# Performance work log

Hardware: AMD Instinct MI355X
Metric: run time of the kernel (lower is better)

## Reference

```python
import jax, jax.numpy as jnp
import numpy as np

B, S, D = 2, 2048, 2048
H = 16
Q_LORA, KV_LORA = 1536, 512
D_NOPE, D_ROPE, D_V = 128, 64, 128
QK_D = D_NOPE + D_ROPE  # 192
EPS = 1e-6
ROPE_THETA = 10000.0


def rms_norm(x, w, eps=EPS):
    return x * jax.lax.rsqrt(jnp.mean(x * x, axis=-1, keepdims=True) + eps) * w


def apply_rope(x, cos, sin):
    # x: [b, s, h, d]; cos/sin: [s, d//2]; pairs are interleaved (x0,x1),(x2,x3),...
    xr, xi = x[..., 0::2], x[..., 1::2]
    c = cos[None, :, None, :]
    s = sin[None, :, None, :]
    yr = xr * c - xi * s
    yi = xr * s + xi * c
    return jnp.stack([yr, yi], axis=-1).reshape(x.shape)


def setup_inputs() -> dict:
    key = jax.random.key(0)
    ks = jax.random.split(key, 8)
    sd = 0.02
    pos = jnp.arange(S, dtype=jnp.float32)
    inv_freq = 1.0 / (ROPE_THETA ** (jnp.arange(0, D_ROPE, 2, dtype=jnp.float32) / D_ROPE))
    ang = pos[:, None] * inv_freq[None, :]  # [S, D_ROPE//2]
    mask = jnp.triu(jnp.full((S, S), float('-inf'), dtype=jnp.float32), k=1)
    return {
        'x': jax.random.normal(ks[0], (B, S, D), dtype=jnp.float32),
        'freqs_cos': jnp.cos(ang),
        'freqs_sin': jnp.sin(ang),
        'mask': mask,
        'wq_a': jax.random.normal(ks[1], (Q_LORA, D), dtype=jnp.float32) * sd,
        'q_norm_w': jnp.ones((Q_LORA,), dtype=jnp.float32),
        'wq_b': jax.random.normal(ks[2], (H * QK_D, Q_LORA), dtype=jnp.float32) * sd,
        'wkv_a': jax.random.normal(ks[3], (KV_LORA + D_ROPE, D), dtype=jnp.float32) * sd,
        'kv_norm_w': jnp.ones((KV_LORA,), dtype=jnp.float32),
        'wkv_b': jax.random.normal(ks[4], (H * (D_NOPE + D_V), KV_LORA), dtype=jnp.float32) * sd,
        'wo': jax.random.normal(ks[5], (D, H * D_V), dtype=jnp.float32) * sd,
    }


def reference(x, freqs_cos, freqs_sin, mask, wq_a, q_norm_w, wq_b, wkv_a, kv_norm_w, wkv_b, wo):
    b, s, _ = x.shape
    # query path: down-proj -> RMSNorm -> up-proj
    q = rms_norm(x @ wq_a.T, q_norm_w) @ wq_b.T          # [b, s, H*QK_D]
    q = q.reshape(b, s, H, QK_D)
    q_nope, q_pe = q[..., :D_NOPE], q[..., D_NOPE:]
    q_pe = apply_rope(q_pe, freqs_cos, freqs_sin)
    # kv path: joint down-proj, split latent / rope key
    kv_full = x @ wkv_a.T                                 # [b, s, KV_LORA + D_ROPE]
    kv, k_pe = kv_full[..., :KV_LORA], kv_full[..., KV_LORA:]
    k_pe = apply_rope(k_pe[:, :, None, :], freqs_cos, freqs_sin)  # [b, s, 1, D_ROPE]
    q = jnp.concatenate([q_nope, q_pe], axis=-1)          # [b, s, H, QK_D]
    kv = rms_norm(kv, kv_norm_w) @ wkv_b.T                # [b, s, H*(D_NOPE+D_V)]
    kv = kv.reshape(b, s, H, D_NOPE + D_V)
    k_nope, v = kv[..., :D_NOPE], kv[..., D_NOPE:]
    k = jnp.concatenate([k_nope, jnp.broadcast_to(k_pe, (b, s, H, D_ROPE))], axis=-1)
    scale = QK_D ** -0.5
    scores = jnp.einsum('bshd,bthd->bsht', q, k) * scale + mask[None, :, None, :]
    probs = jax.nn.softmax(scores.astype(jnp.float32), axis=-1).astype(x.dtype)
    out = jnp.einsum('bsht,bthd->bshd', probs, v).reshape(b, s, H * D_V)
    return out @ wo.T
```

## Files before the change

### kernel.cpp

```cpp
#include <hip/hip_runtime.h>
#include <hip/hip_bf16.h>

typedef __bf16 bf16_t;
typedef __bf16 bf16x8 __attribute__((ext_vector_type(8)));
typedef __bf16 bf16x4 __attribute__((ext_vector_type(4)));
typedef __bf16 bf16x2 __attribute__((ext_vector_type(2)));
typedef float  f32x4  __attribute__((ext_vector_type(4)));
typedef float  f32x16 __attribute__((ext_vector_type(16)));

#define NB 2
#define NS 2048
#define ND 2048
#define NH 16
#define QLORA 1536
#define KVLORA 512
#define DNOPE 128
#define DROPE 64
#define DVDIM 128
#define QKD 192

#define QSCALE 0.10411754f

#if __has_builtin(__builtin_amdgcn_exp2f)
#define EXP2F(x) __builtin_amdgcn_exp2f(x)
#else
#define EXP2F(x) __expf((x) * 0.69314718056f)
#endif
#if __has_builtin(__builtin_amdgcn_rcpf)
#define RCPF(x) __builtin_amdgcn_rcpf(x)
#else
#define RCPF(x) (1.0f / (x))
#endif

typedef __attribute__((address_space(3))) void as3_void;
typedef __attribute__((address_space(1))) const void as1_void;
__device__ __forceinline__ void gload16(const void* g, void* l) {
  __builtin_amdgcn_global_load_lds((as1_void*)g, (as3_void*)l, 16, 0, 0);
}

__device__ __forceinline__ int pack2(float a, float b) {
  bf16x2 t = {(bf16_t)a, (bf16_t)b};
  return __builtin_bit_cast(int, t);
}

__global__ __launch_bounds__(256) void k_cvt_all(
    const float* __restrict__ x, const float* __restrict__ wqa,
    const float* __restrict__ wqb, const float* __restrict__ wkva,
    const float* __restrict__ wkvb, const float* __restrict__ wo,
    bf16_t* __restrict__ xb, bf16_t* __restrict__ wqab, bf16_t* __restrict__ wqbb,
    bf16_t* __restrict__ wkvab, bf16_t* __restrict__ wkvbb, bf16_t* __restrict__ wob) {
  const int c0 = 2097152, c1 = 2883584, c2 = 4063232, c3 = 4358144, c4 = 4882432,
            c5 = 5931008;
  int i = blockIdx.x * 256 + threadIdx.x;
  for (; i < c5; i += gridDim.x * 256) {
    const float* src;
    bf16_t* dst;
    int off;
    if (i < c0) { src = x; dst = xb; off = i; }
    else if (i < c1) { src = wqa; dst = wqab; off = i - c0; }
    else if (i < c2) { src = wqb; dst = wqbb; off = i - c1; }
    else if (i < c3) { src = wkva; dst = wkvab; off = i - c2; }
    else if (i < c4) { src = wkvb; dst = wkvbb; off = i - c3; }
    else { src = wo; dst = wob; off = i - c4; }
    float4 v = reinterpret_cast<const float4*>(src)[off];
    bf16x4 o = {(bf16_t)v.x, (bf16_t)v.y, (bf16_t)v.z, (bf16_t)v.w};
    reinterpret_cast<bf16x4*>(dst)[off] = o;
  }
}

template <int EPI>
__device__ __forceinline__ void gemm_core(
    int rank, bf16_t* As, bf16_t* Bs,
    const bf16_t* __restrict__ A, const bf16_t* __restrict__ Bw,
    float* __restrict__ Cf, float* __restrict__ Cf2,
    bf16_t* __restrict__ Kout, bf16_t* __restrict__ Vtout,
    const float* __restrict__ fc, const float* __restrict__ fs,
    int M, int N, int K) {
  const int tid = threadIdx.x;
  const int lane = tid & 63;
  const int wave = tid >> 6;
  const int wm = (wave >> 1) * 64, wn = (wave & 1) * 64;
  const int nxt = (N + 127) >> 7;
  const int by = rank / nxt, bx = rank - by * nxt;
  const int m0 = by * 128, n0 = bx * 128;
  const int l15 = lane & 15, l4 = lane >> 4;
  const int srow = lane >> 3;
  const int scol = ((lane & 7) ^ srow) * 8;

  const f32x4 Z4 = {0.f, 0.f, 0.f, 0.f};
  f32x4 acc[4][4];
#pragma unroll
  for (int i = 0; i < 4; ++i)
#pragma unroll
    for (int j = 0; j < 4; ++j) acc[i][j] = Z4;

  auto stage = [&](int buf, int k0) {
#pragma unroll
    for (int c = 0; c < 4; ++c) {
      int chunk = c * 4 + wave;
      int row = chunk * 8 + srow;
      gload16(A + (size_t)(m0 + row) * K + k0 + scol, &As[buf * 8192 + chunk * 512]);
      gload16(Bw + (size_t)(n0 + row) * K + k0 + scol, &Bs[buf * 8192 + chunk * 512]);
    }
  };

  const int nk = K >> 6;
  stage(0, 0);
  int cur = 0;
#pragma unroll 1
  for (int t = 0; t < nk; ++t) {
    if (t + 1 < nk) {
      stage(cur ^ 1, (t + 1) * 64);
      asm volatile("s_waitcnt vmcnt(8)" ::: "memory");
    } else {
      asm volatile("s_waitcnt vmcnt(0)" ::: "memory");
    }
    __builtin_amdgcn_sched_barrier(0);
    __builtin_amdgcn_s_barrier();
    __builtin_amdgcn_sched_barrier(0);
#pragma unroll
    for (int ks = 0; ks < 2; ++ks) {
      int kc = ks * 4 + l4;
      int pc = (kc ^ (l15 & 7)) * 8;
      bf16x8 af[4], bfr[4];
#pragma unroll
      for (int f = 0; f < 4; ++f) {
        af[f] = *reinterpret_cast<const bf16x8*>(
            &As[cur * 8192 + (wm + f * 16 + l15) * 64 + pc]);
        bfr[f] = *reinterpret_cast<const bf16x8*>(
            &Bs[cur * 8192 + (wn + f * 16 + l15) * 64 + pc]);
      }
#pragma unroll
      for (int fi = 0; fi < 4; ++fi)
#pragma unroll
        for (int fj = 0; fj < 4; ++fj)
          acc[fi][fj] = __builtin_amdgcn_mfma_f32_16x16x32_bf16(af[fi], bfr[fj], acc[fi][fj], 0, 0, 0);
    }
    __builtin_amdgcn_sched_barrier(0);
    __builtin_amdgcn_s_barrier();
    cur ^= 1;
  }

#pragma unroll
  for (int fi = 0; fi < 4; ++fi) {
#pragma unroll
    for (int fj = 0; fj < 4; ++fj) {
      int col = n0 + wn + fj * 16 + l15;
      int row0 = m0 + wm + fi * 16 + l4 * 4;
      if (EPI == 1) {
        int h = col >> 8, rr = col & 255;
        int b = row0 >> 11, s0 = row0 & 2047;
        if (rr < DNOPE) {
#pragma unroll
          for (int r = 0; r < 4; ++r)
            Kout[(((size_t)(b * NH + h)) * NS + s0 + r) * QKD + rr] =
                (bf16_t)acc[fi][fj][r];
        } else {
          bf16x4 pv4 = {(bf16_t)acc[fi][fj][0], (bf16_t)acc[fi][fj][1],
                        (bf16_t)acc[fi][fj][2], (bf16_t)acc[fi][fj][3]};
          *reinterpret_cast<bf16x4*>(
              &Vtout[(((size_t)(b * NH + h)) * DVDIM + (rr - DNOPE)) * NS + s0]) = pv4;
        }
      } else {
#pragma unroll
        for (int r = 0; r < 4; ++r) {
          int row = row0 + r;
          float v = acc[fi][fj][r];
          if (EPI == 0) {
            Cf[(size_t)row * N + col] = v;
          } else if (EPI == 2) {
            int h = col / 192;
            int d = col - h * 192;
            int b = row >> 11, s = row & 2047;
            float y = v;
            if (d >= DNOPE) {
              float pv = __shfl_xor(v, 1);
              int pp = ((d & ~1) - DNOPE) >> 1;
              float c = fc[s * 32 + pp], si = fs[s * 32 + pp];
              y = (col & 1) ? (pv * si + v * c) : (v * c - pv * si);
            }
            Kout[((size_t)(b * NH + h) * NS + s) * QKD + d] = (bf16_t)(y * QSCALE);
          } else {
            if (col < QLORA) Cf[(size_t)row * QLORA + col] = v;
            else if (col < QLORA + KVLORA + DROPE)
              Cf2[(size_t)row * (KVLORA + DROPE) + (col - QLORA)] = v;
          }
        }
      }
    }
  }
}

template <int EPI>
__global__ __launch_bounds__(256) void k_gemm_bt(
    const bf16_t* __restrict__ A, const bf16_t* __restrict__ Bw,
    float* __restrict__ Cf, float* __restrict__ Cf2,
    bf16_t* __restrict__ Kout, bf16_t* __restrict__ Vtout,
    const float* __restrict__ fc, const float* __restrict__ fs,
    int M, int N, int K) {
  __shared__ bf16_t As[2 * 128 * 64];
  __shared__ bf16_t Bs[2 * 128 * 64];
  const int per = gridDim.x >> 3;
  const int rank = (blockIdx.x & 7) * per + (blockIdx.x >> 3);
  gemm_core<EPI>(rank, As, Bs, A, Bw, Cf, Cf2, Kout, Vtout, fc, fs, M, N, K);
}

__global__ __launch_bounds__(256) void k_gemm_dual(
    const bf16_t* __restrict__ A2, const bf16_t* __restrict__ B2,
    bf16_t* __restrict__ Qb, const float* __restrict__ fc,
    const float* __restrict__ fs, const bf16_t* __restrict__ A1,
    const bf16_t* __restrict__ B1, bf16_t* __restrict__ Kout,
    bf16_t* __restrict__ Vtout) {
  __shared__ bf16_t As[2 * 128 * 64];
  __shared__ bf16_t Bs[2 * 128 * 64];
  const int G2 = 768;
  if ((int)blockIdx.x < G2) {
    int id = blockIdx.x;
    int rank = (id & 7) * (G2 >> 3) + (id >> 3);
    gemm_core<2>(rank, As, Bs, A2, B2, nullptr, nullptr, Qb, nullptr, fc, fs,
                 NB * NS, NH * QKD, QLORA);
  } else {
    int id = blockIdx.x - G2;
    int rank = (id & 7) * (1024 >> 3) + (id >> 3);
    gemm_core<1>(rank, As, Bs, A1, B1, nullptr, nullptr, Kout, Vtout, nullptr,
                 nullptr, NB * NS, NH * (DNOPE + DVDIM), KVLORA);
  }
}

__global__ __launch_bounds__(256) void k_norm_post(
    const float* __restrict__ qa, const float* __restrict__ qw,
    bf16_t* __restrict__ qan, const float* __restrict__ kvf,
    const float* __restrict__ kw, const float* __restrict__ fc,
    const float* __restrict__ fs, bf16_t* __restrict__ kvn,
    bf16_t* __restrict__ Kb) {
  int row = blockIdx.x;
  __shared__ float red[4];
  {
    const float* rp = qa + (size_t)row * QLORA;
    float ss = 0.f;
    for (int c = threadIdx.x * 4; c < QLORA; c += 1024) {
      float4 v = *reinterpret_cast<const float4*>(rp + c);
      ss += v.x * v.x + v.y * v.y + v.z * v.z + v.w * v.w;
    }
#pragma unroll
    for (int m = 32; m; m >>= 1) ss += __shfl_xor(ss, m);
    if ((threadIdx.x & 63) == 0) red[threadIdx.x >> 6] = ss;
    __syncthreads();
    float tot = red[0] + red[1] + red[2] + red[3];
    float rs = rsqrtf(tot / (float)QLORA + 1e-6f);
    for (int c = threadIdx.x * 4; c < QLORA; c += 1024) {
      float4 v = *reinterpret_cast<const float4*>(rp + c);
      bf16x4 o = {(bf16_t)(v.x * rs * qw[c]), (bf16_t)(v.y * rs * qw[c + 1]),
                  (bf16_t)(v.z * rs * qw[c + 2]), (bf16_t)(v.w * rs * qw[c + 3])};
      *reinterpret_cast<bf16x4*>(qan + (size_t)row * QLORA + c) = o;
    }
  }
  __syncthreads();
  const float* rp = kvf + (size_t)row * (KVLORA + DROPE);
  float ss = 0.f;
  float4 v = {0.f, 0.f, 0.f, 0.f};
  if (threadIdx.x < 128) {
    v = reinterpret_cast<const float4*>(rp)[threadIdx.x];
    ss = v.x * v.x + v.y * v.y + v.z * v.z + v.w * v.w;
  }
#pragma unroll
  for (int m = 32; m; m >>= 1) ss += __shfl_xor(ss, m);
  if ((threadIdx.x & 63) == 0) red[threadIdx.x >> 6] = ss;
  __syncthreads();
  float tot = red[0] + red[1] + red[2] + red[3];
  float rs = rsqrtf(tot / (float)KVLORA + 1e-6f);
  if (threadIdx.x < 128) {
    int c = threadIdx.x * 4;
    bf16x4 o = {(bf16_t)(v.x * rs * kw[c]), (bf16_t)(v.y * rs * kw[c + 1]),
                (bf16_t)(v.z * rs * kw[c + 2]), (bf16_t)(v.w * rs * kw[c + 3])};
    *reinterpret_cast<bf16x4*>(kvn + (size_t)row * KVLORA + c) = o;
  }
  int b = row >> 11, s = row & 2047;
  if (threadIdx.x < 32) {
    int p = threadIdx.x;
    float x0 = rp[KVLORA + 2 * p], x1 = rp[KVLORA + 2 * p + 1];
    float c = fc[s * 32 + p], si = fs[s * 32 + p];
    float yr = x0 * c - x1 * si, yi = x0 * si + x1 * c;
    bf16_t br = (bf16_t)yr, bi = (bf16_t)yi;
    for (int h = 0; h < NH; ++h) {
      size_t ob = ((size_t)(b * NH + h) * NS + s) * QKD + DNOPE;
      Kb[ob + 2 * p] = br;
      Kb[ob + 2 * p + 1] = bi;
    }
  }
}

__global__ __launch_bounds__(256, 2) void k_attn(const bf16_t* __restrict__ Qb,
                                                 const bf16_t* __restrict__ Kb,
                                                 const bf16_t* __restrict__ Vtb,
                                                 bf16_t* __restrict__ Ao) {
  __shared__ bf16x8 Ks8[2][64 * 24];
  __shared__ bf16x8 Vs8[2][128 * 8];
  const int id = blockIdx.x;
  const int bh = id & 31;
  const int aa = (id >> 5) & 7;
  const int qt = (id >> 8) ? aa : (15 - aa);
  const int b = bh >> 4, h = bh & 15;
  const int tid = threadIdx.x;
  const int lane = tid & 63, wave = tid >> 6;
  const int l31 = lane & 31, hi = lane >> 5;
  const int q0w = qt * 128 + wave * 32;
  const int qg = q0w + l31;
  const int c4 = hi * 4;
  const int ntiles = 2 * qt + 2;
  const size_t bhNS = (size_t)bh * NS;

  const bf16_t* KbB = Kb + bhNS * QKD;
  const bf16_t* VtB = Vtb + (size_t)bh * DVDIM * NS;
  int koff[6], voff[4];
#pragma unroll
  for (int i = 0; i < 6; ++i) {
    int p = tid + i * 256;
    int row = p / 24, pc = p % 24;
    int lc = (pc & ~7) | ((pc ^ row) & 7);
    koff[i] = row * QKD + lc * 8;
  }
#pragma unroll
  for (int i = 0; i < 4; ++i) {
    int p = tid + i * 256;
    int row = p >> 3, pc = p & 7;
    int lc = pc ^ (row & 7);
    voff[i] = row * NS + lc * 8;
  }

  auto stageKV = [&](int buf, int kv0) {
    const bf16_t* ksrc = KbB + kv0 * QKD;
    const bf16_t* vsrc = VtB + kv0;
    bf16x8* kdst = &Ks8[buf][wave * 64];
    bf16x8* vdst = &Vs8[buf][wave * 64];
#pragma unroll
    for (int i = 0; i < 6; ++i) gload16(ksrc + koff[i], kdst + i * 256);
#pragma unroll
    for (int i = 0; i < 4; ++i) gload16(vsrc + voff[i], vdst + i * 256);
  };

  bf16x8 qf[12];
  {
    const bf16_t* qp = Qb + (bhNS + qg) * QKD + hi * 8;
#pragma unroll
    for (int ks = 0; ks < 12; ++ks)
      qf[ks] = *reinterpret_cast<const bf16x8*>(qp + ks * 16);
  }

  f32x16 oacc[4];
#pragma unroll
  for (int d = 0; d < 4; ++d) oacc[d] = {};
  float mrun = -3e38f, lrun = 0.f;

  stageKV(0, 0);
  int cur = 0;

#pragma unroll 1
  for (int kt = 0; kt < ntiles; ++kt) {
    const int kv0 = kt * 64;
    if (kt + 1 < ntiles) {
      stageKV(cur ^ 1, kv0 + 64);
      asm volatile("s_waitcnt vmcnt(10)" ::: "memory");
    } else {
      asm volatile("s_waitcnt vmcnt(0)" ::: "memory");
    }
    __builtin_amdgcn_sched_barrier(0);
    __builtin_amdgcn_s_barrier();
    __builtin_amdgcn_sched_barrier(0);

    if (kv0 <= q0w + 31) {
      f32x16 sacc[2];
      sacc[0] = {};
      sacc[1] = {};
#pragma unroll
      for (int ks = 0; ks < 12; ++ks) {
#pragma unroll
        for (int kh = 0; kh < 2; ++kh) {
          int row = kh * 32 + l31;
          int c = ks * 2 + hi;
          int pc = (c & ~7) | ((c ^ row) & 7);
          sacc[kh] = __builtin_amdgcn_mfma_f32_32x32x16_bf16(Ks8[cur][row * 24 + pc],
                                                             qf[ks], sacc[kh], 0, 0, 0);
        }
      }

      const bool diag = (kv0 + 63 > q0w);
      float mloc = -3e38f;
#pragma unroll
      for (int kh = 0; kh < 2; ++kh)
#pragma unroll
        for (int rg = 0; rg < 16; ++rg) {
          float s = sacc[kh][rg];
          if (diag) {
            int kg = kv0 + kh * 32 + (rg & 3) + 8 * (rg >> 2) + c4;
            if (kg > qg) s = -3e38f;
            sacc[kh][rg] = s;
          }
          mloc = fmaxf(mloc, s);
        }
      mloc = fmaxf(mloc, __shfl_xor(mloc, 32));

      if (!__all(mloc <= mrun)) {
        float mn = fmaxf(mrun, mloc);
        float fac = EXP2F(mrun - mn);
        mrun = mn;
        lrun *= fac;
#pragma unroll
        for (int d = 0; d < 4; ++d)
#pragma unroll
          for (int rg = 0; rg < 16; ++rg) oacc[d][rg] *= fac;
      }

      float rsum = 0.f;
      int W[8][2];
#pragma unroll
      for (int kh = 0; kh < 2; ++kh)
#pragma unroll
        for (int g = 0; g < 4; ++g) {
          float p0 = EXP2F(sacc[kh][4 * g + 0] - mrun);
          float p1 = EXP2F(sacc[kh][4 * g + 1] - mrun);
          float p2 = EXP2F(sacc[kh][4 * g + 2] - mrun);
          float p3 = EXP2F(sacc[kh][4 * g + 3] - mrun);
          rsum += (p0 + p1) + (p2 + p3);
          W[kh * 4 + g][0] = pack2(p0, p1);
          W[kh * 4 + g][1] = pack2(p2, p3);
        }
      rsum += __shfl_xor(rsum, 32);
      lrun += rsum;

      bf16x8 pa[4];
#pragma unroll
      for (int pks = 0; pks < 4; ++pks) {
        int kh = pks >> 1, G0 = (pks & 1) * 2;
        int a0 = W[kh * 4 + G0][0], a1 = W[kh * 4 + G0][1];
        int b0 = W[kh * 4 + G0 + 1][0], b1 = W[kh * 4 + G0 + 1][1];
        int own0 = hi ? b0 : a0, own1 = hi ? b1 : a1;
        int oth0 = hi ? a0 : b0, oth1 = hi ? a1 : b1;
        int rc0 = __shfl_xor(oth0, 32), rc1 = __shfl_xor(oth1, 32);
        int4 wv;
        wv.x = hi ? rc0 : own0;
        wv.y = hi ? rc1 : own1;
        wv.z = hi ? own0 : rc0;
        wv.w = hi ? own1 : rc1;
        pa[pks] = __builtin_bit_cast(bf16x8, wv);
      }

#pragma unroll
      for (int pks = 0; pks < 4; ++pks)
#pragma unroll
        for (int dvt = 0; dvt < 4; ++dvt) {
          int row = dvt * 32 + l31;
          int pc = (pks * 2 + hi) ^ (row & 7);
          oacc[dvt] = __builtin_amdgcn_mfma_f32_32x32x16_bf16(Vs8[cur][row * 8 + pc],
                                                              pa[pks], oacc[dvt], 0, 0, 0);
        }
    }

    __builtin_amdgcn_sched_barrier(0);
    __builtin_amdgcn_s_barrier();
    cur ^= 1;
  }

  float lr = RCPF(lrun);
  bf16_t* base = Ao + ((size_t)(b * NS) + qg) * (NH * DVDIM) + h * DVDIM;
#pragma unroll
  for (int dvt = 0; dvt < 4; ++dvt)
#pragma unroll
    for (int rg4 = 0; rg4 < 4; ++rg4) {
      int dv0 = dvt * 32 + 8 * rg4 + c4;
      bf16x4 o = {(bf16_t)(oacc[dvt][rg4 * 4 + 0] * lr),
                  (bf16_t)(oacc[dvt][rg4 * 4 + 1] * lr),
                  (bf16_t)(oacc[dvt][rg4 * 4 + 2] * lr),
                  (bf16_t)(oacc[dvt][rg4 * 4 + 3] * lr)};
      *reinterpret_cast<bf16x4*>(base + dv0) = o;
    }
}

extern "C" void kernel_launch(void* const* d_in, const int* in_sizes, int n_in,
                              void* d_out, int out_size, void* d_ws, size_t ws_size,
                              hipStream_t stream) {
  (void)in_sizes; (void)n_in; (void)out_size; (void)ws_size;
  const float* x = (const float*)d_in[0];
  const float* fcos = (const float*)d_in[1];
  const float* fsin = (const float*)d_in[2];
  const float* wq_a = (const float*)d_in[4];
  const float* q_norm_w = (const float*)d_in[5];
  const float* wq_b = (const float*)d_in[6];
  const float* wkv_a = (const float*)d_in[7];
  const float* kv_norm_w = (const float*)d_in[8];
  const float* wkv_b = (const float*)d_in[9];
  const float* wo = (const float*)d_in[10];
  float* out = (float*)d_out;

  char* p = (char*)d_ws;
  bf16_t* x_bf = (bf16_t*)(p);
  bf16_t* wqa_bf = (bf16_t*)(p + 16777216);
  bf16_t* wkva_bf = (bf16_t*)(p + 23068672);
  bf16_t* wqb_bf = (bf16_t*)(p + 25427968);
  bf16_t* wkvb_bf = (bf16_t*)(p + 34865152);
  bf16_t* wo_bf = (bf16_t*)(p + 39059456);
  float* qa_f32 = (float*)(p + 47448064);
  bf16_t* Kb = (bf16_t*)(p + 47448064);
  bf16_t* qan_bf = (bf16_t*)(p + 72613888);
  bf16_t* Qb = (bf16_t*)(p + 85196800);
  char* r2 = p + 110362624;
  float* kvf_f32 = (float*)(r2);
  bf16_t* kvn_bf = (bf16_t*)(r2 + 9437184);
  bf16_t* Vtb = (bf16_t*)(r2 + 13631488);
  bf16_t* attn_bf = (bf16_t*)(r2 + 30408704);

  k_cvt_all<<<2048, 256, 0, stream>>>(x, wq_a, wq_b, wkv_a, wkv_b, wo, x_bf, wqa_bf,
                                      wqb_bf, wkva_bf, wkvb_bf, wo_bf);

  k_gemm_bt<3><<<dim3(544), 256, 0, stream>>>(x_bf, wqa_bf, qa_f32, kvf_f32,
                                              nullptr, nullptr, nullptr, nullptr,
                                              NB * NS, QLORA + KVLORA + DROPE, ND);
  k_norm_post<<<NB * NS, 256, 0, stream>>>(qa_f32, q_norm_w, qan_bf, kvf_f32,
                                           kv_norm_w, fcos, fsin, kvn_bf, Kb);
  k_gemm_dual<<<dim3(1792), 256, 0, stream>>>(qan_bf, wqb_bf, Qb, fcos, fsin,
                                              kvn_bf, wkvb_bf, Kb, Vtb);
  k_attn<<<dim3(512), 256, 0, stream>>>(Qb, Kb, Vtb, attn_bf);
  k_gemm_bt<0><<<dim3(512), 256, 0, stream>>>(attn_bf, wo_bf, out, nullptr, nullptr,
                                              nullptr, nullptr, nullptr, NB * NS, ND,
                                              NH * DVDIM);
}
```

Baseline: 321.2 us.

## Use 256x128 tiles with 512-thread blocks for the dual up-projection GEMM

Adds a gemm_core256 variant that computes 256x128 output tiles with 8 waves, each keeping a 64x64 accumulator, and moves the existing epilogue into a shared gemm_epi helper. k_gemm_dual now launches 896 blocks of 512 threads instead of 1792 blocks of 256. Each B tile loaded into shared memory is reused across twice as many rows, which halves the B-operand global and LDS traffic per output. In exchange the block uses 48KB of LDS and needs more threads per block, which may lower occupancy and leaves fewer blocks to balance across the CUs.

```diff
diff --git a/kernel.cpp b/kernel.cpp
--- a/kernel.cpp
+++ b/kernel.cpp
@@ -69,6 +69,52 @@
 }
 
 template <int EPI>
+__device__ __forceinline__ void gemm_epi(
+    int col, int row0, const f32x4& a4,
+    float* __restrict__ Cf, float* __restrict__ Cf2,
+    bf16_t* __restrict__ Kout, bf16_t* __restrict__ Vtout,
+    const float* __restrict__ fc, const float* __restrict__ fs, int N) {
+  if (EPI == 1) {
+    int h = col >> 8, rr = col & 255;
+    int b = row0 >> 11, s0 = row0 & 2047;
+    if (rr < DNOPE) {
+#pragma unroll
+      for (int r = 0; r < 4; ++r)
+        Kout[(((size_t)(b * NH + h)) * NS + s0 + r) * QKD + rr] = (bf16_t)a4[r];
+    } else {
+      bf16x4 pv4 = {(bf16_t)a4[0], (bf16_t)a4[1], (bf16_t)a4[2], (bf16_t)a4[3]};
+      *reinterpret_cast<bf16x4*>(
+          &Vtout[(((size_t)(b * NH + h)) * DVDIM + (rr - DNOPE)) * NS + s0]) = pv4;
+    }
+  } else {
+#pragma unroll
+    for (int r = 0; r < 4; ++r) {
+      int row = row0 + r;
+      float v = a4[r];
+      if (EPI == 0) {
+        Cf[(size_t)row * N + col] = v;
+      } else if (EPI == 2) {
+        int h = col / 192;
+        int d = col - h * 192;
+        int b = row >> 11, s = row & 2047;
+        float y = v;
+        if (d >= DNOPE) {
+          float pv = __shfl_xor(v, 1);
+          int pp = ((d & ~1) - DNOPE) >> 1;
+          float c = fc[s * 32 + pp], si = fs[s * 32 + pp];
+          y = (col & 1) ? (pv * si + v * c) : (v * c - pv * si);
+        }
+        Kout[((size_t)(b * NH + h) * NS + s) * QKD + d] = (bf16_t)(y * QSCALE);
+      } else {
+        if (col < QLORA) Cf[(size_t)row * QLORA + col] = v;
+        else if (col < QLORA + KVLORA + DROPE)
+          Cf2[(size_t)row * (KVLORA + DROPE) + (col - QLORA)] = v;
+      }
+    }
+  }
+}
+
+template <int EPI>
 __device__ __forceinline__ void gemm_core(
     int rank, bf16_t* As, bf16_t* Bs,
     const bf16_t* __restrict__ A, const bf16_t* __restrict__ Bw,
@@ -142,53 +188,97 @@
   }
 
 #pragma unroll
-  for (int fi = 0; fi < 4; ++fi) {
-#pragma unroll
-    for (int fj = 0; fj < 4; ++fj) {
-      int col = n0 + wn + fj * 16 + l15;
-      int row0 = m0 + wm + fi * 16 + l4 * 4;
-      if (EPI == 1) {
-        int h = col >> 8, rr = col & 255;
-        int b = row0 >> 11, s0 = row0 & 2047;
-        if (rr < DNOPE) {
-#pragma unroll
-          for (int r = 0; r < 4; ++r)
-            Kout[(((size_t)(b * NH + h)) * NS + s0 + r) * QKD + rr] =
-                (bf16_t)acc[fi][fj][r];
-        } else {
-          bf16x4 pv4 = {(bf16_t)acc[fi][fj][0], (bf16_t)acc[fi][fj][1],
-                        (bf16_t)acc[fi][fj][2], (bf16_t)acc[fi][fj][3]};
-          *reinterpret_cast<bf16x4*>(
-              &Vtout[(((size_t)(b * NH + h)) * DVDIM + (rr - DNOPE)) * NS + s0]) = pv4;
-        }
-      } else {
-#pragma unroll
-        for (int r = 0; r < 4; ++r) {
-          int row = row0 + r;
-          float v = acc[fi][fj][r];
-          if (EPI == 0) {
-            Cf[(size_t)row * N + col] = v;
-          } else if (EPI == 2) {
-            int h = col / 192;
-            int d = col - h * 192;
-            int b = row >> 11, s = row & 2047;
-            float y = v;
-            if (d >= DNOPE) {
-              float pv = __shfl_xor(v, 1);
-              int pp = ((d & ~1) - DNOPE) >> 1;
-              float c = fc[s * 32 + pp], si = fs[s * 32 + pp];
-              y = (col & 1) ? (pv * si + v * c) : (v * c - pv * si);
-            }
-            Kout[((size_t)(b * NH + h) * NS + s) * QKD + d] = (bf16_t)(y * QSCALE);
-          } else {
-            if (col < QLORA) Cf[(size_t)row * QLORA + col] = v;
-            else if (col < QLORA + KVLORA + DROPE)
-              Cf2[(size_t)row * (KVLORA + DROPE) + (col - QLORA)] = v;
-          }
-        }
+  for (int fi = 0; fi < 4; ++fi)
+#pragma unroll
+    for (int fj = 0; fj < 4; ++fj)
+      gemm_epi<EPI>(n0 + wn + fj * 16 + l15, m0 + wm + fi * 16 + l4 * 4, acc[fi][fj],
+                    Cf, Cf2, Kout, Vtout, fc, fs, N);
+}
+
+template <int EPI>
+__device__ __forceinline__ void gemm_core256(
+    int rank, bf16_t* As, bf16_t* Bs,
+    const bf16_t* __restrict__ A, const bf16_t* __restrict__ Bw,
+    bf16_t* __restrict__ Kout, bf16_t* __restrict__ Vtout,
+    const float* __restrict__ fc, const float* __restrict__ fs,
+    int N, int K) {
+  const int tid = threadIdx.x;
+  const int lane = tid & 63;
+  const int wave = tid >> 6;
+  const int wm = (wave >> 1) * 64;
+  const int wn = (wave & 1) * 64;
+  const int nxt = N >> 7;
+  const int by = rank / nxt, bx = rank - by * nxt;
+  const int m0 = by * 256, n0 = bx * 128;
+  const int l15 = lane & 15, l4 = lane >> 4;
+  const int srow = lane >> 3;
+  const int scol = ((lane & 7) ^ srow) * 8;
+
+  const f32x4 Z4 = {0.f, 0.f, 0.f, 0.f};
+  f32x4 acc[4][4];
+#pragma unroll
+  for (int i = 0; i < 4; ++i)
+#pragma unroll
+    for (int j = 0; j < 4; ++j) acc[i][j] = Z4;
+
+  auto stage = [&](int buf, int k0) {
+#pragma unroll
+    for (int a = 0; a < 4; ++a) {
+      int chunk = a * 8 + wave;
+      int row = chunk * 8 + srow;
+      gload16(A + (size_t)(m0 + row) * K + k0 + scol, &As[buf * 16384 + chunk * 512]);
+    }
+#pragma unroll
+    for (int bq = 0; bq < 2; ++bq) {
+      int chunk = bq * 8 + wave;
+      int row = chunk * 8 + srow;
+      gload16(Bw + (size_t)(n0 + row) * K + k0 + scol, &Bs[buf * 8192 + chunk * 512]);
+    }
+  };
+
+  const int nk = K >> 6;
+  stage(0, 0);
+  int cur = 0;
+#pragma unroll 1
+  for (int t = 0; t < nk; ++t) {
+    if (t + 1 < nk) {
+      stage(cur ^ 1, (t + 1) * 64);
+      asm volatile("s_waitcnt vmcnt(6)" ::: "memory");
+    } else {
+      asm volatile("s_waitcnt vmcnt(0)" ::: "memory");
+    }
+    __builtin_amdgcn_sched_barrier(0);
+    __builtin_amdgcn_s_barrier();
+    __builtin_amdgcn_sched_barrier(0);
+#pragma unroll
+    for (int ks = 0; ks < 2; ++ks) {
+      int kc = ks * 4 + l4;
+      int pc = (kc ^ (l15 & 7)) * 8;
+      bf16x8 af[4], bfr[4];
+#pragma unroll
+      for (int f = 0; f < 4; ++f) {
+        af[f] = *reinterpret_cast<const bf16x8*>(
+            &As[cur * 16384 + (wm + f * 16 + l15) * 64 + pc]);
+        bfr[f] = *reinterpret_cast<const bf16x8*>(
+            &Bs[cur * 8192 + (wn + f * 16 + l15) * 64 + pc]);
       }
-    }
-  }
+#pragma unroll
+      for (int fi = 0; fi < 4; ++fi)
+#pragma unroll
+        for (int fj = 0; fj < 4; ++fj)
+          acc[fi][fj] = __builtin_amdgcn_mfma_f32_16x16x32_bf16(af[fi], bfr[fj], acc[fi][fj], 0, 0, 0);
+    }
+    __builtin_amdgcn_sched_barrier(0);
+    __builtin_amdgcn_s_barrier();
+    cur ^= 1;
+  }
+
+#pragma unroll
+  for (int fi = 0; fi < 4; ++fi)
+#pragma unroll
+    for (int fj = 0; fj < 4; ++fj)
+      gemm_epi<EPI>(n0 + wn + fj * 16 + l15, m0 + wm + fi * 16 + l4 * 4, acc[fi][fj],
+                    nullptr, nullptr, Kout, Vtout, fc, fs, N);
 }
 
 template <int EPI>
@@ -205,25 +295,24 @@
   gemm_core<EPI>(rank, As, Bs, A, Bw, Cf, Cf2, Kout, Vtout, fc, fs, M, N, K);
 }
 
-__global__ __launch_bounds__(256) void k_gemm_dual(
+__global__ __launch_bounds__(512) void k_gemm_dual(
     const bf16_t* __restrict__ A2, const bf16_t* __restrict__ B2,
     bf16_t* __restrict__ Qb, const float* __restrict__ fc,
     const float* __restrict__ fs, const bf16_t* __restrict__ A1,
     const bf16_t* __restrict__ B1, bf16_t* __restrict__ Kout,
     bf16_t* __restrict__ Vtout) {
-  __shared__ bf16_t As[2 * 128 * 64];
+  __shared__ bf16_t As[2 * 256 * 64];
   __shared__ bf16_t Bs[2 * 128 * 64];
-  const int G2 = 768;
+  const int G2 = 384;
   if ((int)blockIdx.x < G2) {
     int id = blockIdx.x;
     int rank = (id & 7) * (G2 >> 3) + (id >> 3);
-    gemm_core<2>(rank, As, Bs, A2, B2, nullptr, nullptr, Qb, nullptr, fc, fs,
-                 NB * NS, NH * QKD, QLORA);
+    gemm_core256<2>(rank, As, Bs, A2, B2, Qb, nullptr, fc, fs, NH * QKD, QLORA);
   } else {
     int id = blockIdx.x - G2;
-    int rank = (id & 7) * (1024 >> 3) + (id >> 3);
-    gemm_core<1>(rank, As, Bs, A1, B1, nullptr, nullptr, Kout, Vtout, nullptr,
-                 nullptr, NB * NS, NH * (DNOPE + DVDIM), KVLORA);
+    int rank = (id & 7) * 64 + (id >> 3);
+    gemm_core256<1>(rank, As, Bs, A1, B1, Kout, Vtout, nullptr, nullptr,
+                    NH * (DNOPE + DVDIM), KVLORA);
   }
 }
 
@@ -517,8 +606,8 @@
                                               NB * NS, QLORA + KVLORA + DROPE, ND);
   k_norm_post<<<NB * NS, 256, 0, stream>>>(qa_f32, q_norm_w, qan_bf, kvf_f32,
                                            kv_norm_w, fcos, fsin, kvn_bf, Kb);
-  k_gemm_dual<<<dim3(1792), 256, 0, stream>>>(qan_bf, wqb_bf, Qb, fcos, fsin,
-                                              kvn_bf, wkvb_bf, Kb, Vtb);
+  k_gemm_dual<<<dim3(896), 512, 0, stream>>>(qan_bf, wqb_bf, Qb, fcos, fsin,
+                                             kvn_bf, wkvb_bf, Kb, Vtb);
   k_attn<<<dim3(512), 256, 0, stream>>>(Qb, Kb, Vtb, attn_bf);
   k_gemm_bt<0><<<dim3(512), 256, 0, stream>>>(attn_bf, wo_bf, out, nullptr, nullptr,
                                               nullptr, nullptr, nullptr, NB * NS, ND,
```

Result: slower. 333.1 us (+3.7%).
